# Kernel optimization log

Measured on AMD Instinct MI355X. Metric: run time of the kernel, lower is better.

## Reference

```python
import jax, jax.numpy as jnp
import numpy as np

N_NODES = 20000
N_EDGES = 200000
N_GRAPHS = 128
EMB = 256
N_LAYERS = 4
NUM_ELEMENTS = 84
RBF_DIM = 10
RBF_CUTOFF = 8.0


def setup_inputs() -> dict:
    key = jax.random.key(0)
    ks = jax.random.split(key, 20)
    inp = {
        'x': jax.random.randint(ks[0], (N_NODES, 1), 0, NUM_ELEMENTS, dtype=jnp.int64) if jax.config.read('jax_enable_x64') else jax.random.randint(ks[0], (N_NODES, 1), 0, NUM_ELEMENTS).astype(jnp.int32),
        'src': jax.random.randint(ks[1], (N_EDGES,), 0, N_NODES).astype(jnp.int32),
        'dst': jax.random.randint(ks[2], (N_EDGES,), 0, N_NODES).astype(jnp.int32),
        'e': jax.random.uniform(ks[3], (N_EDGES, 1), dtype=jnp.float32) * RBF_CUTOFF,
        'i': jnp.sort(jax.random.randint(ks[4], (N_NODES,), 0, N_GRAPHS)).astype(jnp.int32),
    }
    s_emb = 1.0 / np.sqrt(EMB)
    # element embedding table
    inp['emb_table'] = jax.random.normal(ks[5], (NUM_ELEMENTS, EMB), jnp.float32) * s_emb
    # dense_e applied to RBF expansion
    inp['We'] = jax.random.normal(ks[6], (RBF_DIM, EMB), jnp.float32) * (1.0 / np.sqrt(RBF_DIM))
    inp['be'] = jnp.zeros((EMB,), jnp.float32)
    # CGCNN-style gated message passing layers (stacked over layers)
    def w(k):
        return jax.random.normal(k, (N_LAYERS, EMB, EMB), jnp.float32) * s_emb
    inp['Wg_x'] = w(ks[7]); inp['Wg_n'] = w(ks[8]); inp['Wg_e'] = w(ks[9])
    inp['bg'] = jnp.zeros((N_LAYERS, EMB), jnp.float32)
    inp['Wf_x'] = w(ks[10]); inp['Wf_n'] = w(ks[11]); inp['Wf_e'] = w(ks[12])
    inp['bf'] = jnp.zeros((N_LAYERS, EMB), jnp.float32)
    # dense_n: embedding -> 12
    inp['Wn'] = jax.random.normal(ks[13], (EMB, 12), jnp.float32) * s_emb
    inp['bn'] = jnp.zeros((12,), jnp.float32)
    return inp


def _rbf_expand(d):
    # Gaussian radial basis expansion of scalar distances: [E] -> [E, RBF_DIM]
    centers = jnp.linspace(0.0, RBF_CUTOFF, RBF_DIM, dtype=d.dtype)
    width = centers[1] - centers[0]
    return jnp.exp(-(((d[:, None] - centers) / width) ** 2))


def reference(x, src, dst, e, i, emb_table, We, be, Wg_x, Wg_n, Wg_e, bg,
              Wf_x, Wf_n, Wf_e, bf, Wn, bn):
    xn = emb_table[x[:, 0]]                     # [N, EMB] element embedding
    ef = _rbf_expand(e[:, 0]) @ We + be         # [E, EMB] edge features
    for l in range(N_LAYERS):
        h_i = xn[dst]                           # receiver node features [E, EMB]
        h_j = xn[src]                           # sender node features   [E, EMB]
        # gate/filter computed as split matmuls (equivalent to Dense on concat)
        zg = h_i @ Wg_x[l] + h_j @ Wg_n[l] + ef @ Wg_e[l] + bg[l]
        zf = h_i @ Wf_x[l] + h_j @ Wf_n[l] + ef @ Wf_e[l] + bf[l]
        msg = jax.nn.sigmoid(zg) * jax.nn.softplus(zf)   # [E, EMB]
        agg = jax.ops.segment_sum(msg, dst, num_segments=N_NODES)
        xn = agg + xn                           # residual add (in model call)
    xs = xn @ Wn + bn                           # [N, 12]
    sums = jax.ops.segment_sum(xs, i, num_segments=N_GRAPHS)
    cnts = jax.ops.segment_sum(jnp.ones((xs.shape[0], 1), xs.dtype), i,
                               num_segments=N_GRAPHS)
    out = sums / jnp.maximum(cnts, 1.0)         # global average pool per graph
    return out.reshape(N_GRAPHS, 3, 4)
```

## Files before the change

### kernel.cpp

```cpp
#include <hip/hip_runtime.h>
#include <hip/hip_bf16.h>
#include <math.h>

#define NN   20000
#define NE   200000
#define NG   128
#define EMBD 256
#define NL   4
#define RBFD 10
#define TBINS 2048
#define NWAVE 8192
#define GSPL 8

typedef __attribute__((ext_vector_type(8))) short bf16x8;
typedef __attribute__((ext_vector_type(4))) float f32x4;

__device__ __forceinline__ f32x4 up4(uint2 u) {
  f32x4 r;
  r.x = __uint_as_float(u.x << 16);
  r.y = __uint_as_float(u.x & 0xffff0000u);
  r.z = __uint_as_float(u.y << 16);
  r.w = __uint_as_float(u.y & 0xffff0000u);
  return r;
}

__device__ __forceinline__ void gload16(const void* g, void* l) {
  __builtin_amdgcn_global_load_lds(
      (const __attribute__((address_space(1))) void*)g,
      (__attribute__((address_space(3))) void*)l, 16, 0, 0);
}

__device__ __forceinline__ unsigned short bfbits(float v) {
  __hip_bfloat16 h = __float2bfloat16(v);
  return *(unsigned short*)&h;
}


__global__ void k_embed(const int* __restrict__ x, const float* __restrict__ emb,
                        float* __restrict__ xn, __hip_bfloat16* __restrict__ xnb) {
  int idx = blockIdx.x * blockDim.x + threadIdx.x;
  if (idx >= NN * (EMBD / 4)) return;
  int n  = idx >> 6;
  int c4 = (idx & 63) << 2;
  float4 v = *(const float4*)(emb + (size_t)x[n] * EMBD + c4);
  *(float4*)(xn + (size_t)n * EMBD + c4) = v;
  __hip_bfloat16* xb = xnb + (size_t)n * EMBD + c4;
  xb[0] = __float2bfloat16(v.x); xb[1] = __float2bfloat16(v.y);
  xb[2] = __float2bfloat16(v.z); xb[3] = __float2bfloat16(v.w);
}

__global__ void k_wsmall(const float* __restrict__ We, const float* __restrict__ be,
                         const float* __restrict__ Wge, const float* __restrict__ bg,
                         const float* __restrict__ Wfe, const float* __restrict__ bf,
                         float* __restrict__ weff, float* __restrict__ beff) {
  int tid = blockIdx.x * blockDim.x + threadIdx.x;
  const int WPER = RBFD * EMBD;
  if (tid < NL * 2 * WPER) {
    int l  = tid / (2 * WPER);
    int r  = tid % (2 * WPER);
    int gf = r / WPER;
    int r2 = r % WPER;
    int k = r2 / EMBD, c = r2 % EMBD;
    const float* W = (gf == 0 ? Wge : Wfe) + (size_t)l * EMBD * EMBD;
    float s = 0.f;
    for (int j = 0; j < EMBD; ++j) s += We[k * EMBD + j] * W[(size_t)j * EMBD + c];
    weff[tid] = s;
  } else {
    int t2 = tid - NL * 2 * WPER;
    if (t2 >= NL * 2 * EMBD) return;
    int l  = t2 / (2 * EMBD);
    int r  = t2 % (2 * EMBD);
    int gf = r / EMBD, c = r % EMBD;
    const float* W = (gf == 0 ? Wge : Wfe) + (size_t)l * EMBD * EMBD;
    const float* b = (gf == 0 ? bg : bf) + (size_t)l * EMBD;
    float s = b[c];
    for (int j = 0; j < EMBD; ++j) s += be[j] * W[(size_t)j * EMBD + c];
    beff[t2] = s;
  }
}

__global__ void k_table(const float* __restrict__ weff, const float* __restrict__ beff,
                        __hip_bfloat16* __restrict__ tbl) {
  int idx = blockIdx.x * blockDim.x + threadIdx.x;
  if (idx >= NL * (TBINS + 1) * 512) return;
  int l = idx / ((TBINS + 1) * 512);
  int r = idx % ((TBINS + 1) * 512);
  int bin = r >> 9;
  int t = r & 511;
  int gf = t >> 8, c = t & 255;
  float d = (float)bin * (8.0f / (float)TBINS);
  const float* w = weff + ((size_t)(l * 2 + gf) * RBFD) * EMBD + c;
  float s = beff[(size_t)(l * 2 + gf) * EMBD + c];
  const float width = 8.0f / 9.0f;
  #pragma unroll
  for (int k = 0; k < RBFD; ++k) {
    float u = (d - (float)k * width) / width;
    s += __expf(-u * u) * w[(size_t)k * EMBD];
  }
  tbl[idx] = __float2bfloat16(s);
}

__global__ __launch_bounds__(256) void k_wprep(
    const float* __restrict__ Wgx, const float* __restrict__ Wfx,
    const float* __restrict__ Wgn, const float* __restrict__ Wfn,
    __hip_bfloat16* __restrict__ WT) {
  __shared__ float T[64][65];
  int lq = blockIdx.x; int l = lq >> 2, q = lq & 3;
  const float* W = (q == 0 ? Wgx : q == 1 ? Wfx : q == 2 ? Wgn : Wfn) + (size_t)l * 65536;
  int t = blockIdx.y;
  int k0 = (t & 3) * 64, c0 = (t >> 2) * 64;
  #pragma unroll
  for (int i = 0; i < 16; ++i) {
    int idx = threadIdx.x + i * 256;
    int r = idx >> 6, c = idx & 63;
    T[r][c] = W[(size_t)(k0 + r) * 256 + c0 + c];
  }
  __syncthreads();
  __hip_bfloat16* out = WT + ((size_t)lq * 256) * 256;
  #pragma unroll
  for (int i = 0; i < 16; ++i) {
    int idx = threadIdx.x + i * 256;
    int r = idx >> 6, c = idx & 63;
    out[(size_t)(c0 + r) * 256 + k0 + c] = __float2bfloat16(T[c][r]);
  }
}


__global__ void k_hist(const int* __restrict__ dst, int* __restrict__ cnt) {
  int e = blockIdx.x * blockDim.x + threadIdx.x;
  if (e >= NE) return;
  atomicAdd(&cnt[dst[e]], 1);
}

__global__ __launch_bounds__(1024) void k_scan(const int* __restrict__ cnt,
                                               int* __restrict__ roff,
                                               int* __restrict__ cursor) {
  __shared__ int part[1024];
  const int t = threadIdx.x;
  const int CH = 20;
  int base = t * CH;
  int loc[CH];
  int s = 0;
  #pragma unroll
  for (int i = 0; i < CH; ++i) {
    int idx = base + i;
    int v = (idx < NN) ? cnt[idx] : 0;
    loc[i] = s;
    s += v;
  }
  part[t] = s;
  __syncthreads();
  for (int off = 1; off < 1024; off <<= 1) {
    int v = (t >= off) ? part[t - off] : 0;
    __syncthreads();
    part[t] += v;
    __syncthreads();
  }
  int chunkbase = (t == 0) ? 0 : part[t - 1];
  #pragma unroll
  for (int i = 0; i < CH; ++i) {
    int idx = base + i;
    if (idx < NN) {
      int v = chunkbase + loc[i];
      roff[idx] = v;
      cursor[idx] = v;
    }
  }
  if (t == 1023) roff[NN] = part[1023];
}

__global__ void k_scatter(const int* __restrict__ src, const int* __restrict__ dst,
                          const float* __restrict__ edist,
                          int* __restrict__ cursor,
                          int* __restrict__ src_s, int* __restrict__ bin_s) {
  int e = blockIdx.x * blockDim.x + threadIdx.x;
  if (e >= NE) return;
  int d = dst[e];
  int p = atomicAdd(&cursor[d], 1);
  src_s[p] = src[e];
  int bin = (int)(edist[e] * ((float)TBINS / 8.0f) + 0.5f);
  bin = bin < 0 ? 0 : (bin > TBINS ? TBINS : bin);
  bin_s[p] = bin << 9;
}


__global__ __launch_bounds__(256) void k_nodemm(
    const __hip_bfloat16* __restrict__ xnb, const __hip_bfloat16* __restrict__ WTl,
    __hip_bfloat16* __restrict__ Yb) {
  __shared__ unsigned short As[128 * 64];
  __shared__ unsigned short Bs[128 * 64];
  const int tid = threadIdx.x;
  const int lane = tid & 63;
  const int wave = tid >> 6;
  const int row0 = blockIdx.x << 7;
  const int col0 = blockIdx.y << 7;
  const int q = col0 >> 8;
  const int cb = col0 & 255;
  const unsigned short* xb = (const unsigned short*)xnb;
  const unsigned short* Wb = (const unsigned short*)WTl + ((size_t)q * 256 + cb) * 256;
  const int wnode = (wave >> 1) << 6;
  const int wch   = (wave & 1) << 6;
  f32x4 acc[4][4] = {};

  const int rd0 = (wave << 3) + (lane >> 3);
  const int cd  = lane & 7;

  for (int k0 = 0; k0 < 256; k0 += 64) {
    #pragma unroll
    for (int j = 0; j < 4; ++j) {
      int rd = rd0 + j * 32;
      int cs = cd ^ (rd & 7);
      int ga = row0 + rd; if (ga > NN - 1) ga = NN - 1;
      gload16(xb + (size_t)ga * 256 + k0 + cs * 8,
              (char*)As + (size_t)(j * 256 + wave * 64) * 16);
      gload16(Wb + (size_t)rd * 256 + k0 + cs * 8,
              (char*)Bs + (size_t)(j * 256 + wave * 64) * 16);
    }
    __syncthreads();
    const int rsel = lane & 15, ksl = lane >> 4;
    #pragma unroll
    for (int h = 0; h < 2; ++h) {
      const int c = h * 4 + ksl;
      bf16x8 xa[4], wf[4];
      #pragma unroll
      for (int nn = 0; nn < 4; ++nn) {
        int r = wnode + nn * 16 + rsel;
        xa[nn] = *(const bf16x8*)(&As[r * 64 + (c ^ (r & 7)) * 8]);
      }
      #pragma unroll
      for (int mc = 0; mc < 4; ++mc) {
        int r = wch + mc * 16 + rsel;
        wf[mc] = *(const bf16x8*)(&Bs[r * 64 + (c ^ (r & 7)) * 8]);
      }
      #pragma unroll
      for (int mc = 0; mc < 4; ++mc)
        #pragma unroll
        for (int nn = 0; nn < 4; ++nn)
          acc[mc][nn] = __builtin_amdgcn_mfma_f32_16x16x32_bf16(wf[mc], xa[nn], acc[mc][nn], 0, 0, 0);
    }
    __syncthreads();
  }

  const int nodesel = lane & 15;
  const int chq = (lane >> 4) << 2;
  #pragma unroll
  for (int mc = 0; mc < 4; ++mc) {
    #pragma unroll
    for (int nn = 0; nn < 4; ++nn) {
      int node = row0 + wnode + nn * 16 + nodesel;
      if (node < NN) {
        int ch = col0 + wch + mc * 16 + chq;
        ushort4 pk;
        pk.x = bfbits(acc[mc][nn][0]);
        pk.y = bfbits(acc[mc][nn][1]);
        pk.z = bfbits(acc[mc][nn][2]);
        pk.w = bfbits(acc[mc][nn][3]);
        *(ushort4*)((unsigned short*)Yb + (size_t)node * 1024 + ch) = pk;
      }
    }
  }
}

__device__ __forceinline__ float gate1(float zg, float zf) {
  float sg = __builtin_amdgcn_rcpf(1.0f + __expf(-zg));
  float sp = fmaxf(zf, 0.0f) + __logf(1.0f + __expf(-fabsf(zf)));
  return sg * sp;
}

__global__ __launch_bounds__(256, 8) void k_agg(
    const __hip_bfloat16* __restrict__ Yb, const int* __restrict__ roff,
    const int* __restrict__ src_s, const int* __restrict__ bin_s,
    const __hip_bfloat16* __restrict__ tblL,
    float* __restrict__ xn, __hip_bfloat16* __restrict__ xnb) {
  const int wave = threadIdx.x >> 6, lane = threadIdx.x & 63;
  const int c4 = lane << 2;
  const int wid0 = blockIdx.x * 4 + wave;
  const unsigned short* Ybu = (const unsigned short*)Yb;
  const unsigned short* Tbu = (const unsigned short*)tblL;

  for (int n = wid0; n < NN; n += NWAVE) {
    const int jb   = __builtin_amdgcn_readfirstlane(roff[n]);
    const int jend = __builtin_amdgcn_readfirstlane(roff[n + 1]);
    const int deg = jend - jb;

    const unsigned short* yr = Ybu + (size_t)n * 1024;
    f32x4 bgv = up4(*(const uint2*)(yr + c4));
    f32x4 bfv = up4(*(const uint2*)(yr + c4 + 256));

    f32x4 m4 = {};
    if (deg > 0) {
      const int dcap = deg < 64 ? deg : 64;
      int sv = 0, bv = 0;
      if (lane < dcap) {
        sv = src_s[jb + lane];
        bv = bin_s[jb + lane];
      }
      for (int i = 0; i < dcap; ++i) {
        int sn = __builtin_amdgcn_readlane(sv, i);
        int bo = __builtin_amdgcn_readlane(bv, i);
        const unsigned short* ys = Ybu + (size_t)sn * 1024 + 512;
        uint2 pa = *(const uint2*)(ys + c4);
        uint2 pf = *(const uint2*)(ys + c4 + 256);
        const unsigned short* tp = Tbu + bo;
        uint2 tg = *(const uint2*)(tp + c4);
        uint2 tf = *(const uint2*)(tp + c4 + 256);
        f32x4 zg = bgv + up4(pa) + up4(tg);
        f32x4 zf = bfv + up4(pf) + up4(tf);
        m4.x += gate1(zg.x, zf.x);
        m4.y += gate1(zg.y, zf.y);
        m4.z += gate1(zg.z, zf.z);
        m4.w += gate1(zg.w, zf.w);
      }
      for (int i = 64; i < deg; ++i) {
        int sn = src_s[jb + i];
        int bo = bin_s[jb + i];
        const unsigned short* ys = Ybu + (size_t)sn * 1024 + 512;
        uint2 pa = *(const uint2*)(ys + c4);
        uint2 pf = *(const uint2*)(ys + c4 + 256);
        const unsigned short* tp = Tbu + bo;
        uint2 tg = *(const uint2*)(tp + c4);
        uint2 tf = *(const uint2*)(tp + c4 + 256);
        f32x4 zg = bgv + up4(pa) + up4(tg);
        f32x4 zf = bfv + up4(pf) + up4(tf);
        m4.x += gate1(zg.x, zf.x);
        m4.y += gate1(zg.y, zf.y);
        m4.z += gate1(zg.z, zf.z);
        m4.w += gate1(zg.w, zf.w);
      }
    }
    float4 xv = *(const float4*)(xn + (size_t)n * EMBD + c4);
    xv.x += m4.x; xv.y += m4.y; xv.z += m4.z; xv.w += m4.w;
    *(float4*)(xn + (size_t)n * EMBD + c4) = xv;
    __hip_bfloat16* xbp = xnb + (size_t)n * EMBD + c4;
    xbp[0] = __float2bfloat16(xv.x); xbp[1] = __float2bfloat16(xv.y);
    xbp[2] = __float2bfloat16(xv.z); xbp[3] = __float2bfloat16(xv.w);
  }
}


__global__ __launch_bounds__(256) void k_gsum(
    const float* __restrict__ xn, const int* __restrict__ gi,
    float* __restrict__ gpart, float* __restrict__ gcnt) {
  const int g = blockIdx.x, p = blockIdx.y;
  int lo = 0, hi = NN;
  while (lo < hi) { int m = (lo + hi) >> 1; if (gi[m] < g) lo = m + 1; else hi = m; }
  int lo2 = lo, hi2 = NN;
  while (lo2 < hi2) { int m = (lo2 + hi2) >> 1; if (gi[m] < g + 1) lo2 = m + 1; else hi2 = m; }
  const int cntv = lo2 - lo;
  const int r0 = lo + (cntv * p) / GSPL;
  const int r1 = lo + (cntv * (p + 1)) / GSPL;
  const int c = threadIdx.x;
  float acc = 0.f;
  for (int r = r0; r < r1; ++r) acc += xn[(size_t)r * EMBD + c];
  gpart[((size_t)g * GSPL + p) * EMBD + c] = acc;
  if (p == 0 && c == 0) gcnt[g] = (float)cntv;
}

__global__ __launch_bounds__(256) void k_final(
    const float* __restrict__ gpart, const float* __restrict__ gcnt,
    const float* __restrict__ Wn, const float* __restrict__ bn,
    float* __restrict__ out) {
  __shared__ float s[EMBD];
  const int g = blockIdx.x;
  const int c = threadIdx.x;
  float v = 0.f;
  #pragma unroll
  for (int p = 0; p < GSPL; ++p) v += gpart[((size_t)g * GSPL + p) * EMBD + c];
  s[c] = v;
  __syncthreads();
  if (c < 12) {
    float acc = 0.f;
    for (int k = 0; k < EMBD; ++k) acc += s[k] * Wn[k * 12 + c];
    float cv = gcnt[g];
    out[g * 12 + c] = (cv > 0.f) ? acc / cv + bn[c] : 0.f;
  }
}


extern "C" void kernel_launch(void* const* d_in, const int* in_sizes, int n_in,
                              void* d_out, int out_size, void* d_ws, size_t ws_size,
                              hipStream_t stream) {
  const int*   x   = (const int*)d_in[0];
  const int*   src = (const int*)d_in[1];
  const int*   dst = (const int*)d_in[2];
  const float* e   = (const float*)d_in[3];
  const int*   gi  = (const int*)d_in[4];
  const float* emb = (const float*)d_in[5];
  const float* We  = (const float*)d_in[6];
  const float* be  = (const float*)d_in[7];
  const float* Wgx = (const float*)d_in[8];
  const float* Wgn = (const float*)d_in[9];
  const float* Wge = (const float*)d_in[10];
  const float* bg  = (const float*)d_in[11];
  const float* Wfx = (const float*)d_in[12];
  const float* Wfn = (const float*)d_in[13];
  const float* Wfe = (const float*)d_in[14];
  const float* bf  = (const float*)d_in[15];
  const float* Wn  = (const float*)d_in[16];
  const float* bn  = (const float*)d_in[17];
  float* out = (float*)d_out;

  char* ws = (char*)d_ws;
  size_t off = 0;
  auto alloc = [&](size_t bytes) {
    void* p = ws + off;
    off += (bytes + 255) & ~(size_t)255;
    return p;
  };
  float*           xn    = (float*)alloc((size_t)NN * EMBD * 4);
  __hip_bfloat16*  xnb   = (__hip_bfloat16*)alloc((size_t)NN * EMBD * 2);
  __hip_bfloat16*  Yb    = (__hip_bfloat16*)alloc((size_t)NN * 1024 * 2);
  int*             bin_s = (int*)alloc((size_t)NE * 4);
  int*             src_s = (int*)alloc((size_t)NE * 4);
  int*             cnt   = (int*)alloc((size_t)NN * 4);
  int*             roff  = (int*)alloc((size_t)(NN + 1) * 4);
  int*             curs  = (int*)alloc((size_t)NN * 4);
  float*           weff  = (float*)alloc((size_t)NL * 2 * RBFD * EMBD * 4);
  float*           beff  = (float*)alloc((size_t)NL * 2 * EMBD * 4);
  __hip_bfloat16*  tbl   = (__hip_bfloat16*)alloc((size_t)NL * (TBINS + 1) * 512 * 2);
  __hip_bfloat16*  WT    = (__hip_bfloat16*)alloc((size_t)NL * 4 * 256 * 256 * 2);
  float*           gpart = (float*)alloc((size_t)NG * GSPL * EMBD * 4);
  float*           gcnt  = (float*)alloc((size_t)NG * 4);
  (void)ws_size; (void)in_sizes; (void)n_in; (void)out_size;

  hipMemsetAsync(cnt, 0, (size_t)NN * 4, stream);

  k_embed<<<(NN * (EMBD / 4) + 255) / 256, 256, 0, stream>>>(x, emb, xn, xnb);
  k_wsmall<<<(NL * 2 * (RBFD + 1) * EMBD + 255) / 256, 256, 0, stream>>>(
      We, be, Wge, bg, Wfe, bf, weff, beff);
  k_table<<<(NL * (TBINS + 1) * 512 + 255) / 256, 256, 0, stream>>>(weff, beff, tbl);
  k_wprep<<<dim3(NL * 4, 16), 256, 0, stream>>>(Wgx, Wfx, Wgn, Wfn, WT);
  k_hist<<<(NE + 255) / 256, 256, 0, stream>>>(dst, cnt);
  k_scan<<<1, 1024, 0, stream>>>(cnt, roff, curs);
  k_scatter<<<(NE + 255) / 256, 256, 0, stream>>>(src, dst, e, curs, src_s, bin_s);

  dim3 mmgrid((NN + 127) / 128, 8);
  for (int l = 0; l < NL; ++l) {
    k_nodemm<<<mmgrid, 256, 0, stream>>>(xnb, WT + (size_t)l * 4 * 65536, Yb);
    k_agg<<<NWAVE / 4, 256, 0, stream>>>(
        Yb, roff, src_s, bin_s, tbl + (size_t)l * (TBINS + 1) * 512, xn, xnb);
  }
  k_gsum<<<dim3(NG, GSPL), 256, 0, stream>>>(xn, gi, gpart, gcnt);
  k_final<<<NG, 256, 0, stream>>>(gpart, gcnt, Wn, bn, out);
}
```

Baseline: 477.7 us.

## Load node-GEMM MFMA operands directly from global memory, dropping LDS staging

The node projection GEMM no longer stages A and B tiles in LDS with global_load_lds and barriers. Each lane now loads its bf16x8 MFMA fragments straight from global memory across a fully unrolled K loop, and the launch bounds ask for 4 blocks per CU. This removes shared-memory traffic and synchronisation. The trade-off is redundant global/L2 reads, since fragments are re-fetched by every wave that uses them, and higher register pressure from the unrolling.

```diff
diff --git a/kernel.cpp b/kernel.cpp
--- a/kernel.cpp
+++ b/kernel.cpp
@@ -22,12 +22,6 @@
   r.z = __uint_as_float(u.y << 16);
   r.w = __uint_as_float(u.y & 0xffff0000u);
   return r;
-}
-
-__device__ __forceinline__ void gload16(const void* g, void* l) {
-  __builtin_amdgcn_global_load_lds(
-      (const __attribute__((address_space(1))) void*)g,
-      (__attribute__((address_space(3))) void*)l, 16, 0, 0);
 }
 
 __device__ __forceinline__ unsigned short bfbits(float v) {
@@ -184,14 +178,11 @@
 }
 
 
-__global__ __launch_bounds__(256) void k_nodemm(
+__global__ __launch_bounds__(256, 4) void k_nodemm(
     const __hip_bfloat16* __restrict__ xnb, const __hip_bfloat16* __restrict__ WTl,
     __hip_bfloat16* __restrict__ Yb) {
-  __shared__ unsigned short As[128 * 64];
-  __shared__ unsigned short Bs[128 * 64];
-  const int tid = threadIdx.x;
-  const int lane = tid & 63;
-  const int wave = tid >> 6;
+  const int lane = threadIdx.x & 63;
+  const int wave = threadIdx.x >> 6;
   const int row0 = blockIdx.x << 7;
   const int col0 = blockIdx.y << 7;
   const int q = col0 >> 8;
@@ -200,45 +191,32 @@
   const unsigned short* Wb = (const unsigned short*)WTl + ((size_t)q * 256 + cb) * 256;
   const int wnode = (wave >> 1) << 6;
   const int wch   = (wave & 1) << 6;
+  const int rsel = lane & 15;
+  const int kof  = (lane >> 4) << 3;
+
+  const unsigned short* ab[4];
+  const unsigned short* wb[4];
+  #pragma unroll
+  for (int m = 0; m < 4; ++m) {
+    int ga = row0 + wnode + m * 16 + rsel; if (ga > NN - 1) ga = NN - 1;
+    ab[m] = xb + (size_t)ga * 256 + kof;
+    wb[m] = Wb + (size_t)(wch + m * 16 + rsel) * 256 + kof;
+  }
+
   f32x4 acc[4][4] = {};
-
-  const int rd0 = (wave << 3) + (lane >> 3);
-  const int cd  = lane & 7;
-
-  for (int k0 = 0; k0 < 256; k0 += 64) {
+  #pragma unroll
+  for (int k0 = 0; k0 < 256; k0 += 32) {
+    bf16x8 xa[4], wf[4];
     #pragma unroll
-    for (int j = 0; j < 4; ++j) {
-      int rd = rd0 + j * 32;
-      int cs = cd ^ (rd & 7);
-      int ga = row0 + rd; if (ga > NN - 1) ga = NN - 1;
-      gload16(xb + (size_t)ga * 256 + k0 + cs * 8,
-              (char*)As + (size_t)(j * 256 + wave * 64) * 16);
-      gload16(Wb + (size_t)rd * 256 + k0 + cs * 8,
-              (char*)Bs + (size_t)(j * 256 + wave * 64) * 16);
+    for (int m = 0; m < 4; ++m) {
+      xa[m] = *(const bf16x8*)(ab[m] + k0);
+      wf[m] = *(const bf16x8*)(wb[m] + k0);
     }
-    __syncthreads();
-    const int rsel = lane & 15, ksl = lane >> 4;
     #pragma unroll
-    for (int h = 0; h < 2; ++h) {
-      const int c = h * 4 + ksl;
-      bf16x8 xa[4], wf[4];
+    for (int mc = 0; mc < 4; ++mc)
       #pragma unroll
-      for (int nn = 0; nn < 4; ++nn) {
-        int r = wnode + nn * 16 + rsel;
-        xa[nn] = *(const bf16x8*)(&As[r * 64 + (c ^ (r & 7)) * 8]);
-      }
-      #pragma unroll
-      for (int mc = 0; mc < 4; ++mc) {
-        int r = wch + mc * 16 + rsel;
-        wf[mc] = *(const bf16x8*)(&Bs[r * 64 + (c ^ (r & 7)) * 8]);
-      }
-      #pragma unroll
-      for (int mc = 0; mc < 4; ++mc)
-        #pragma unroll
-        for (int nn = 0; nn < 4; ++nn)
-          acc[mc][nn] = __builtin_amdgcn_mfma_f32_16x16x32_bf16(wf[mc], xa[nn], acc[mc][nn], 0, 0, 0);
-    }
-    __syncthreads();
+      for (int nn = 0; nn < 4; ++nn)
+        acc[mc][nn] = __builtin_amdgcn_mfma_f32_16x16x32_bf16(wf[mc], xa[nn], acc[mc][nn], 0, 0, 0);
   }
 
   const int nodesel = lane & 15;
```

Result: slower. 577.1 us (+20.8%).
